# Kernel optimization log

Hardware: AMD Instinct MI355X
Metric: run time of the kernel (lower is better)

Reference implementation:

```python
import jax, jax.numpy as jnp
import numpy as np

N_NODES = 100000
N_EDGES = 1600000
F_IN = 64
F_HID = 64
F_OUT = 64
N_HEADS = 4


def setup_inputs() -> dict:
    key = jax.random.key(0)
    ks = jax.random.split(key, 7)
    h = jax.random.normal(ks[0], (N_NODES, F_IN), dtype=jnp.float32)
    src = jax.random.randint(ks[1], (N_EDGES,), 0, N_NODES, dtype=jnp.int32)
    dst = jax.random.randint(ks[2], (N_EDGES,), 0, N_NODES, dtype=jnp.int32)
    s = 1.0 / np.sqrt(F_IN)
    Wk = jax.random.normal(ks[3], (F_IN, F_HID), dtype=jnp.float32) * s
    Wq = jax.random.normal(ks[4], (F_IN, F_HID), dtype=jnp.float32) * s
    W = jax.random.normal(ks[5], (F_IN, F_OUT), dtype=jnp.float32) * s
    b = jnp.zeros((F_OUT,), dtype=jnp.float32)
    return {"h": h, "src": src, "dst": dst, "Wk": Wk, "Wq": Wq, "W": W, "b": b,
            "num_heads": N_HEADS}


def reference(h, src, dst, Wk, Wq, W, b, num_heads):
    N = h.shape[0]
    H = num_heads
    # k, q: [N, H, Dh]
    k = (h @ Wk).reshape(N, H, -1)
    q = (h @ Wq).reshape(N, H, -1)
    # edge scores e[e,h] = <k[src], q[dst]>  (u_dot_v)
    e = jnp.einsum('ehd,ehd->eh', k[src], q[dst])  # [E, H]
    # edge softmax over incoming edges of each destination node (per head)
    m = jax.ops.segment_max(e, dst, num_segments=N)          # [N, H]
    m = jax.lax.stop_gradient(m)
    ex = jnp.exp(e - m[dst])                                  # [E, H]
    z = jax.ops.segment_sum(ex, dst, num_segments=N)          # [N, H]
    a = ex / z[dst]                                           # [E, H]
    # message m = u_mul_e(h, a): broadcast (F,) with (H,1) -> [E, H, F]; sum to dst
    msg = h[src][:, None, :] * a[:, :, None]                  # [E, H, F]
    hn = jax.ops.segment_sum(msg, dst, num_segments=N)        # [N, H, F]
    out = hn @ W + b                                          # [N, H, F_out]
    return out.reshape(N, -1)                                 # [N, H*F_out]
```

## Files before the change

### kernel.cpp

```cpp
#include <hip/hip_runtime.h>
#include <hip/hip_fp16.h>
#include <math.h>


#define FDIM 64
#define NHEADS 4
#define TILE 8192
#define BCAP 6144

typedef float f32x2 __attribute__((ext_vector_type(2)));

__global__ __launch_bounds__(256) void k1_kernel(
    const float* __restrict__ h, const float* __restrict__ Wk,
    const float* __restrict__ Wq, const float* __restrict__ Wo,
    const int* __restrict__ src, const int* __restrict__ dst,
    __half* __restrict__ k16, __half* __restrict__ q16,
    __half* __restrict__ hp16, int* __restrict__ gcnt,
    unsigned int* __restrict__ ebuf,
    int N, int E, int KQB, int PB, int nbuck)
{
    __shared__ __align__(16) unsigned char smem_raw[39936];
    int bid = blockIdx.x;
    int t = threadIdx.x;
    if (bid < KQB) {
        float* sWk = (float*)smem_raw;
        float* sWq = (float*)(smem_raw + 16384);
        for (int i = t; i < FDIM * FDIM; i += 256) {
            sWk[i] = Wk[i] * 1.4426950408889634f;
            sWq[i] = Wq[i];
        }
        __syncthreads();
        int cg = t & 3;
        int rg = t >> 2;
        long base = (long)bid * 128 + rg * 2;
        const float4* sWk4 = (const float4*)sWk;
        const float4* sWq4 = (const float4*)sWq;
        const float4* h4 = (const float4*)h;
        float acck[2][16], accq[2][16];
#pragma unroll
        for (int i = 0; i < 2; ++i)
#pragma unroll
            for (int c = 0; c < 16; ++c) { acck[i][c] = 0.f; accq[i][c] = 0.f; }

        for (int fs = 0; fs < FDIM; fs += 4) {
            float4 hv[2];
#pragma unroll
            for (int i = 0; i < 2; ++i) {
                long r = base + i; if (r >= N) r = N - 1;
                hv[i] = h4[r * 16 + (fs >> 2)];
            }
#pragma unroll
            for (int fi = 0; fi < 4; ++fi) {
                int f = fs + fi;
                float4 wk0 = sWk4[f * 16 + cg * 4 + 0];
                float4 wk1 = sWk4[f * 16 + cg * 4 + 1];
                float4 wk2 = sWk4[f * 16 + cg * 4 + 2];
                float4 wk3 = sWk4[f * 16 + cg * 4 + 3];
                float4 wq0 = sWq4[f * 16 + cg * 4 + 0];
                float4 wq1 = sWq4[f * 16 + cg * 4 + 1];
                float4 wq2 = sWq4[f * 16 + cg * 4 + 2];
                float4 wq3 = sWq4[f * 16 + cg * 4 + 3];
#pragma unroll
                for (int i = 0; i < 2; ++i) {
                    float hvf = (&hv[i].x)[fi];
                    acck[i][0]  = fmaf(hvf, wk0.x, acck[i][0]);
                    acck[i][1]  = fmaf(hvf, wk0.y, acck[i][1]);
                    acck[i][2]  = fmaf(hvf, wk0.z, acck[i][2]);
                    acck[i][3]  = fmaf(hvf, wk0.w, acck[i][3]);
                    acck[i][4]  = fmaf(hvf, wk1.x, acck[i][4]);
                    acck[i][5]  = fmaf(hvf, wk1.y, acck[i][5]);
                    acck[i][6]  = fmaf(hvf, wk1.z, acck[i][6]);
                    acck[i][7]  = fmaf(hvf, wk1.w, acck[i][7]);
                    acck[i][8]  = fmaf(hvf, wk2.x, acck[i][8]);
                    acck[i][9]  = fmaf(hvf, wk2.y, acck[i][9]);
                    acck[i][10] = fmaf(hvf, wk2.z, acck[i][10]);
                    acck[i][11] = fmaf(hvf, wk2.w, acck[i][11]);
                    acck[i][12] = fmaf(hvf, wk3.x, acck[i][12]);
                    acck[i][13] = fmaf(hvf, wk3.y, acck[i][13]);
                    acck[i][14] = fmaf(hvf, wk3.z, acck[i][14]);
                    acck[i][15] = fmaf(hvf, wk3.w, acck[i][15]);
                    accq[i][0]  = fmaf(hvf, wq0.x, accq[i][0]);
                    accq[i][1]  = fmaf(hvf, wq0.y, accq[i][1]);
                    accq[i][2]  = fmaf(hvf, wq0.z, accq[i][2]);
                    accq[i][3]  = fmaf(hvf, wq0.w, accq[i][3]);
                    accq[i][4]  = fmaf(hvf, wq1.x, accq[i][4]);
                    accq[i][5]  = fmaf(hvf, wq1.y, accq[i][5]);
                    accq[i][6]  = fmaf(hvf, wq1.z, accq[i][6]);
                    accq[i][7]  = fmaf(hvf, wq1.w, accq[i][7]);
                    accq[i][8]  = fmaf(hvf, wq2.x, accq[i][8]);
                    accq[i][9]  = fmaf(hvf, wq2.y, accq[i][9]);
                    accq[i][10] = fmaf(hvf, wq2.z, accq[i][10]);
                    accq[i][11] = fmaf(hvf, wq2.w, accq[i][11]);
                    accq[i][12] = fmaf(hvf, wq3.x, accq[i][12]);
                    accq[i][13] = fmaf(hvf, wq3.y, accq[i][13]);
                    accq[i][14] = fmaf(hvf, wq3.z, accq[i][14]);
                    accq[i][15] = fmaf(hvf, wq3.w, accq[i][15]);
                }
            }
        }
#pragma unroll
        for (int i = 0; i < 2; ++i) {
            long r = base + i;
            if (r >= N) continue;
            __half2 hk[8], hq[8];
#pragma unroll
            for (int c = 0; c < 8; ++c) {
                hk[c] = __floats2half2_rn(acck[i][2 * c], acck[i][2 * c + 1]);
                hq[c] = __floats2half2_rn(accq[i][2 * c], accq[i][2 * c + 1]);
            }
            float4* kout = (float4*)(k16 + (size_t)r * FDIM + cg * 16);
            float4* qout = (float4*)(q16 + (size_t)r * FDIM + cg * 16);
            kout[0] = ((float4*)hk)[0]; kout[1] = ((float4*)hk)[1];
            qout[0] = ((float4*)hq)[0]; qout[1] = ((float4*)hq)[1];
        }
    } else if (bid < KQB + PB) {
        float* sW = (float*)smem_raw;
        for (int i = t; i < FDIM * FDIM; i += 256) sW[i] = Wo[i];
        __syncthreads();
        int cg = t & 3;
        int rg = t >> 2;
        long base = (long)(bid - KQB) * 128 + rg * 2;
        const float4* sW4 = (const float4*)sW;
        const float4* h4 = (const float4*)h;
        float accp[2][16];
#pragma unroll
        for (int i = 0; i < 2; ++i)
#pragma unroll
            for (int c = 0; c < 16; ++c) accp[i][c] = 0.f;

        for (int fs = 0; fs < FDIM; fs += 4) {
            float4 hv[2];
#pragma unroll
            for (int i = 0; i < 2; ++i) {
                long r = base + i; if (r >= N) r = N - 1;
                hv[i] = h4[r * 16 + (fs >> 2)];
            }
#pragma unroll
            for (int fi = 0; fi < 4; ++fi) {
                int f = fs + fi;
                float4 w0 = sW4[f * 16 + cg * 4 + 0];
                float4 w1 = sW4[f * 16 + cg * 4 + 1];
                float4 w2 = sW4[f * 16 + cg * 4 + 2];
                float4 w3 = sW4[f * 16 + cg * 4 + 3];
#pragma unroll
                for (int i = 0; i < 2; ++i) {
                    float hvf = (&hv[i].x)[fi];
                    accp[i][0]  = fmaf(hvf, w0.x, accp[i][0]);
                    accp[i][1]  = fmaf(hvf, w0.y, accp[i][1]);
                    accp[i][2]  = fmaf(hvf, w0.z, accp[i][2]);
                    accp[i][3]  = fmaf(hvf, w0.w, accp[i][3]);
                    accp[i][4]  = fmaf(hvf, w1.x, accp[i][4]);
                    accp[i][5]  = fmaf(hvf, w1.y, accp[i][5]);
                    accp[i][6]  = fmaf(hvf, w1.z, accp[i][6]);
                    accp[i][7]  = fmaf(hvf, w1.w, accp[i][7]);
                    accp[i][8]  = fmaf(hvf, w2.x, accp[i][8]);
                    accp[i][9]  = fmaf(hvf, w2.y, accp[i][9]);
                    accp[i][10] = fmaf(hvf, w2.z, accp[i][10]);
                    accp[i][11] = fmaf(hvf, w2.w, accp[i][11]);
                    accp[i][12] = fmaf(hvf, w3.x, accp[i][12]);
                    accp[i][13] = fmaf(hvf, w3.y, accp[i][13]);
                    accp[i][14] = fmaf(hvf, w3.z, accp[i][14]);
                    accp[i][15] = fmaf(hvf, w3.w, accp[i][15]);
                }
            }
        }
#pragma unroll
        for (int i = 0; i < 2; ++i) {
            long r = base + i;
            if (r >= N) continue;
            __half2 hp[8];
#pragma unroll
            for (int c = 0; c < 8; ++c)
                hp[c] = __floats2half2_rn(accp[i][2 * c], accp[i][2 * c + 1]);
            float4* pout = (float4*)(hp16 + (size_t)r * FDIM + cg * 16);
            pout[0] = ((float4*)hp)[0];
            pout[1] = ((float4*)hp)[1];
        }
    } else {
        unsigned int* bh     = (unsigned int*)smem_raw;
        unsigned int* bstart = bh + 512;
        unsigned int* bbase  = bstart + 512;
        unsigned int* sd     = bbase + 512;
        unsigned int* ebuf_l = sd + 256;
        long e0 = (long)(bid - KQB - PB) * TILE;
        int cnt_tile = (int)(((long)E - e0 < (long)TILE) ? ((long)E - e0) : (long)TILE);

        bh[t] = 0; bh[t + 256] = 0;
        __syncthreads();
        for (int j = t; j < cnt_tile; j += 256)
            atomicAdd(&bh[dst[e0 + j] >> 8], 1u);
        __syncthreads();
        unsigned int c0 = bh[2 * t], c1 = bh[2 * t + 1];
        unsigned int s = c0 + c1;
        sd[t] = s;
        __syncthreads();
        for (int off = 1; off < 256; off <<= 1) {
            unsigned int v = (t >= off) ? sd[t - off] : 0;
            __syncthreads();
            sd[t] += v;
            __syncthreads();
        }
        unsigned int ex = sd[t] - s;
        bh[2 * t] = ex;          bstart[2 * t] = ex;
        bh[2 * t + 1] = ex + c0; bstart[2 * t + 1] = ex + c0;
        if (c0 > 0) bbase[2 * t] = (unsigned int)atomicAdd(&gcnt[2 * t], (int)c0);
        if (c1 > 0) bbase[2 * t + 1] = (unsigned int)atomicAdd(&gcnt[2 * t + 1], (int)c1);
        __syncthreads();
        for (int j = t; j < cnt_tile; j += 256) {
            int d = dst[e0 + j];
            int sv = src[e0 + j];
            unsigned int pos = atomicAdd(&bh[d >> 8], 1u);
            ebuf_l[pos] = ((unsigned int)sv << 8) | (unsigned int)(d & 255);
        }
        __syncthreads();
        int wave = t >> 6, lane = t & 63;
        for (int b = wave; b < nbuck; b += 4) {
            unsigned int st = bstart[b];
            unsigned int en = bh[b];
            if (st == en) continue;
            unsigned int gb = bbase[b];
            if (gb >= (unsigned int)BCAP) continue;
            unsigned int room = (unsigned int)BCAP - gb;
            if (en - st > room) en = st + room;
            unsigned int* dstp = ebuf + (size_t)b * BCAP + gb;
            for (unsigned int j = st + lane; j < en; j += 64)
                dstp[j - st] = ebuf_l[j];
        }
    }
}

__global__ __launch_bounds__(1024) void binB_kernel(
    const int* __restrict__ gcnt, const unsigned int* __restrict__ ebuf,
    int* __restrict__ rowptr, int* __restrict__ srcs, int N)
{
    __shared__ int sg[512];
    __shared__ unsigned int lh[256];
    __shared__ unsigned int sd[256];
    __shared__ unsigned int ebuf_l[BCAP];
    __shared__ unsigned int srcs_l[BCAP];
    int t = threadIdx.x;
    int b = blockIdx.x;

    int c0 = 0, c1 = 0;
    if (t < 256) {
        c0 = gcnt[2 * t]; c1 = gcnt[2 * t + 1];
        sd[t] = (unsigned int)(c0 + c1);
        lh[t] = 0;
    }
    __syncthreads();
    for (int off = 1; off < 256; off <<= 1) {
        unsigned int v = (t < 256 && t >= off) ? sd[t - off] : 0;
        __syncthreads();
        if (t < 256) sd[t] += v;
        __syncthreads();
    }
    if (t < 256) {
        int ex = (int)sd[t] - (c0 + c1);
        sg[2 * t] = ex;
        sg[2 * t + 1] = ex + c0;
    }
    __syncthreads();
    int gb = sg[b];
    int cnt = gcnt[b];
    if (cnt > BCAP) cnt = BCAP;
    int n0 = b << 8;
    const unsigned int* eb = ebuf + (size_t)b * BCAP;

    for (int j = t; j < cnt; j += 1024) {
        unsigned int p = eb[j];
        ebuf_l[j] = p;
        atomicAdd(&lh[p & 255u], 1u);
    }
    __syncthreads();
    unsigned int c = 0;
    if (t < 256) { c = lh[t]; sd[t] = c; }
    __syncthreads();
    for (int off = 1; off < 256; off <<= 1) {
        unsigned int v = (t < 256 && t >= off) ? sd[t - off] : 0;
        __syncthreads();
        if (t < 256) sd[t] += v;
        __syncthreads();
    }
    if (t < 256) {
        unsigned int excl = sd[t] - c;
        lh[t] = excl;
        if (n0 + t < N) rowptr[n0 + t] = gb + (int)excl;
    }
    __syncthreads();
    for (int j = t; j < cnt; j += 1024) {
        unsigned int p = ebuf_l[j];
        unsigned int pos = atomicAdd(&lh[p & 255u], 1u);
        srcs_l[pos] = p >> 8;
    }
    __syncthreads();
    for (int j = t; j < cnt; j += 1024)
        srcs[gb + j] = (int)srcs_l[j];
}

__device__ __forceinline__ float dot16(const float4* kk, const float* qf) {
    const __half2* kh = (const __half2*)kk;
    float acc = 0.f;
#pragma unroll
    for (int j = 0; j < 8; ++j) {
        float2 kf = __half22float2(kh[j]);
        acc = fmaf(kf.x, qf[2 * j], acc);
        acc = fmaf(kf.y, qf[2 * j + 1], acc);
    }
    return acc;
}

__global__ __launch_bounds__(256) void fused_sa_kernel(
    const int* __restrict__ rowptr, const int* __restrict__ srcs,
    const __half* __restrict__ k16, const __half* __restrict__ q16,
    const __half* __restrict__ hp16, const float* __restrict__ bvec,
    float* __restrict__ out, int N, int E)
{
    int lane = threadIdx.x & 63;
    int n = blockIdx.x * 4 + (threadIdx.x >> 6);
    if (n >= N) return;
    int start = rowptr[n];
    int end   = (n == N - 1) ? E : rowptr[n + 1];

    int hh = lane & 3;
    int rr = lane >> 2;
    int qt = lane >> 4;
    int fq = lane & 15;

    const float4* qp = (const float4*)(q16 + (size_t)n * FDIM + hh * 16);
    float4 qv[2] = { qp[0], qp[1] };
    const __half2* qh = (const __half2*)qv;
    float qf[16];
#pragma unroll
    for (int j = 0; j < 8; ++j) {
        float2 f = __half22float2(qh[j]);
        qf[2 * j] = f.x;
        qf[2 * j + 1] = f.y;
    }

    float zacc = 0.f;
    f32x2 a00 = {0.f,0.f}, a01 = {0.f,0.f};
    f32x2 a10 = {0.f,0.f}, a11 = {0.f,0.f};
    f32x2 a20 = {0.f,0.f}, a21 = {0.f,0.f};
    f32x2 a30 = {0.f,0.f}, a31 = {0.f,0.f};

    for (int base = start; base < end; base += 16) {
        int idx = base + rr;
        bool valid = (idx < end);
        int ic = valid ? idx : (end - 1);
        int sA = srcs[ic];
        int sB0 = __shfl(sA, 4 * qt,      64);
        int sB1 = __shfl(sA, 16 + 4 * qt, 64);
        int sB2 = __shfl(sA, 32 + 4 * qt, 64);
        int sB3 = __shfl(sA, 48 + 4 * qt, 64);
        const float4* kp = (const float4*)(k16 + (size_t)sA * FDIM + hh * 16);
        float4 ka0 = kp[0], ka1 = kp[1];
        uint2 g0 = *(const uint2*)(hp16 + (size_t)sB0 * FDIM + fq * 4);
        uint2 g1 = *(const uint2*)(hp16 + (size_t)sB1 * FDIM + fq * 4);
        uint2 g2 = *(const uint2*)(hp16 + (size_t)sB2 * FDIM + fq * 4);
        uint2 g3 = *(const uint2*)(hp16 + (size_t)sB3 * FDIM + fq * 4);

        float4 ka[2] = { ka0, ka1 };
        float w = __builtin_amdgcn_exp2f(dot16(ka, qf));
        w = valid ? w : 0.f;
        zacc += w;

#define GRP(G, LBASE)                                                      \
    {   float w0 = __shfl(w, (LBASE) + 0, 64);                             \
        float w1 = __shfl(w, (LBASE) + 1, 64);                             \
        float w2 = __shfl(w, (LBASE) + 2, 64);                             \
        float w3 = __shfl(w, (LBASE) + 3, 64);                             \
        float2 flo = __half22float2(*(__half2*)&(G).x);                    \
        float2 fhi = __half22float2(*(__half2*)&(G).y);                    \
        f32x2 vlo; vlo.x = flo.x; vlo.y = flo.y;                           \
        f32x2 vhi; vhi.x = fhi.x; vhi.y = fhi.y;                           \
        f32x2 wv;                                                          \
        wv.x = w0; wv.y = w0;                                              \
        a00 = __builtin_elementwise_fma(wv, vlo, a00);                     \
        a01 = __builtin_elementwise_fma(wv, vhi, a01);                     \
        wv.x = w1; wv.y = w1;                                              \
        a10 = __builtin_elementwise_fma(wv, vlo, a10);                     \
        a11 = __builtin_elementwise_fma(wv, vhi, a11);                     \
        wv.x = w2; wv.y = w2;                                              \
        a20 = __builtin_elementwise_fma(wv, vlo, a20);                     \
        a21 = __builtin_elementwise_fma(wv, vhi, a21);                     \
        wv.x = w3; wv.y = w3;                                              \
        a30 = __builtin_elementwise_fma(wv, vlo, a30);                     \
        a31 = __builtin_elementwise_fma(wv, vhi, a31);                     }

        GRP(g0, 4 * qt)
        if (base + 4 < end)  { GRP(g1, 16 + 4 * qt) }
        if (base + 8 < end)  { GRP(g2, 32 + 4 * qt) }
        if (base + 12 < end) { GRP(g3, 48 + 4 * qt) }
#undef GRP
    }

    zacc += __shfl_xor(zacc, 4, 64);
    zacc += __shfl_xor(zacc, 8, 64);
    zacc += __shfl_xor(zacc, 16, 64);
    zacc += __shfl_xor(zacc, 32, 64);
    float z0 = __shfl(zacc, 0, 64);
    float z1 = __shfl(zacc, 1, 64);
    float z2 = __shfl(zacc, 2, 64);
    float z3 = __shfl(zacc, 3, 64);

#define MQ(A) \
    (A).x += __shfl_xor((A).x, 16, 64); (A).y += __shfl_xor((A).y, 16, 64); \
    (A).x += __shfl_xor((A).x, 32, 64); (A).y += __shfl_xor((A).y, 32, 64);
    MQ(a00) MQ(a01) MQ(a10) MQ(a11) MQ(a20) MQ(a21) MQ(a30) MQ(a31)
#undef MQ

    if (qt != 0) return;
    float4 bv = *(const float4*)(bvec + fq * 4);
    float4* o = (float4*)(out + (size_t)n * (NHEADS * FDIM));
    if (end > start) {
        float rz0 = 1.f / z0;
        float rz1 = 1.f / z1;
        float rz2 = 1.f / z2;
        float rz3 = 1.f / z3;
        o[fq] = make_float4(fmaf(a00.x, rz0, bv.x), fmaf(a00.y, rz0, bv.y),
                            fmaf(a01.x, rz0, bv.z), fmaf(a01.y, rz0, bv.w));
        o[16 + fq] = make_float4(fmaf(a10.x, rz1, bv.x), fmaf(a10.y, rz1, bv.y),
                                 fmaf(a11.x, rz1, bv.z), fmaf(a11.y, rz1, bv.w));
        o[32 + fq] = make_float4(fmaf(a20.x, rz2, bv.x), fmaf(a20.y, rz2, bv.y),
                                 fmaf(a21.x, rz2, bv.z), fmaf(a21.y, rz2, bv.w));
        o[48 + fq] = make_float4(fmaf(a30.x, rz3, bv.x), fmaf(a30.y, rz3, bv.y),
                                 fmaf(a31.x, rz3, bv.z), fmaf(a31.y, rz3, bv.w));
    } else {
        o[fq] = bv; o[16 + fq] = bv; o[32 + fq] = bv; o[48 + fq] = bv;
    }
}

extern "C" void kernel_launch(void* const* d_in, const int* in_sizes, int n_in,
                              void* d_out, int out_size, void* d_ws, size_t ws_size,
                              hipStream_t stream) {
    const float* h   = (const float*)d_in[0];
    const int*   src = (const int*)d_in[1];
    const int*   dst = (const int*)d_in[2];
    const float* Wk  = (const float*)d_in[3];
    const float* Wq  = (const float*)d_in[4];
    const float* W   = (const float*)d_in[5];
    const float* b   = (const float*)d_in[6];
    float* out = (float*)d_out;

    const int N = in_sizes[0] / FDIM;
    const int E = in_sizes[1];

    const int NBUCK = (N + 255) >> 8;
    const int NTILE = (E + TILE - 1) / TILE;
    const int KQB   = (N + 127) / 128;
    const int PB    = (N + 127) / 128;

    __half* k16 = (__half*)d_ws;
    __half* q16 = k16 + (size_t)N * FDIM;
    __half* hp16 = q16 + (size_t)N * FDIM;
    unsigned int* ebuf = (unsigned int*)(hp16 + (size_t)N * FDIM);
    int* srcs   = (int*)(ebuf + (size_t)NBUCK * BCAP);
    int* gcnt   = srcs + E;
    int* rowptr = gcnt + 512;

    hipMemsetAsync(gcnt, 0, 512 * sizeof(int), stream);

    k1_kernel<<<KQB + PB + NTILE, 256, 0, stream>>>(
        h, Wk, Wq, W, src, dst, k16, q16, hp16, gcnt, ebuf,
        N, E, KQB, PB, NBUCK);
    binB_kernel<<<NBUCK, 1024, 0, stream>>>(gcnt, ebuf, rowptr, srcs, N);
    fused_sa_kernel<<<(N + 3) / 4, 256, 0, stream>>>(
        rowptr, srcs, k16, q16, hp16, b, out, N, E);
}
```

Before: 315.0 us.

## Process four destination nodes per wavefront in fused attention kernel

```diff
diff --git a/kernel.cpp b/kernel.cpp
--- a/kernel.cpp
+++ b/kernel.cpp
@@ -316,17 +316,21 @@
     float* __restrict__ out, int N, int E)
 {
     int lane = threadIdx.x & 63;
-    int n = blockIdx.x * 4 + (threadIdx.x >> 6);
-    if (n >= N) return;
-    int start = rowptr[n];
-    int end   = (n == N - 1) ? E : rowptr[n + 1];
-
-    int hh = lane & 3;
-    int rr = lane >> 2;
+    int wid = threadIdx.x >> 6;
     int qt = lane >> 4;
-    int fq = lane & 15;
-
-    const float4* qp = (const float4*)(q16 + (size_t)n * FDIM + hh * 16);
+    int ql = lane & 15;
+    int n = blockIdx.x * 16 + wid * 4 + qt;
+    bool nvalid = (n < N);
+    int nc = nvalid ? n : N - 1;
+    int start = rowptr[nc];
+    int end = (nc == N - 1) ? E : rowptr[nc + 1];
+    if (!nvalid) end = start;
+
+    int rr = ql >> 2;
+    int hh = ql & 3;
+    int qb = qt * 16;
+
+    const float4* qp = (const float4*)(q16 + (size_t)nc * FDIM + hh * 16);
     float4 qv[2] = { qp[0], qp[1] };
     const __half2* qh = (const __half2*)qv;
     float qf[16];
@@ -343,21 +347,21 @@
     f32x2 a20 = {0.f,0.f}, a21 = {0.f,0.f};
     f32x2 a30 = {0.f,0.f}, a31 = {0.f,0.f};
 
-    for (int base = start; base < end; base += 16) {
+    for (int base = start; base < end; base += 4) {
         int idx = base + rr;
         bool valid = (idx < end);
         int ic = valid ? idx : (end - 1);
         int sA = srcs[ic];
-        int sB0 = __shfl(sA, 4 * qt,      64);
-        int sB1 = __shfl(sA, 16 + 4 * qt, 64);
-        int sB2 = __shfl(sA, 32 + 4 * qt, 64);
-        int sB3 = __shfl(sA, 48 + 4 * qt, 64);
+        int s0 = __shfl(sA, qb + 0,  64);
+        int s1 = __shfl(sA, qb + 4,  64);
+        int s2 = __shfl(sA, qb + 8,  64);
+        int s3 = __shfl(sA, qb + 12, 64);
         const float4* kp = (const float4*)(k16 + (size_t)sA * FDIM + hh * 16);
         float4 ka0 = kp[0], ka1 = kp[1];
-        uint2 g0 = *(const uint2*)(hp16 + (size_t)sB0 * FDIM + fq * 4);
-        uint2 g1 = *(const uint2*)(hp16 + (size_t)sB1 * FDIM + fq * 4);
-        uint2 g2 = *(const uint2*)(hp16 + (size_t)sB2 * FDIM + fq * 4);
-        uint2 g3 = *(const uint2*)(hp16 + (size_t)sB3 * FDIM + fq * 4);
+        uint2 g0 = *(const uint2*)(hp16 + (size_t)s0 * FDIM + ql * 4);
+        uint2 g1 = *(const uint2*)(hp16 + (size_t)s1 * FDIM + ql * 4);
+        uint2 g2 = *(const uint2*)(hp16 + (size_t)s2 * FDIM + ql * 4);
+        uint2 g3 = *(const uint2*)(hp16 + (size_t)s3 * FDIM + ql * 4);
 
         float4 ka[2] = { ka0, ka1 };
         float w = __builtin_amdgcn_exp2f(dot16(ka, qf));
@@ -387,46 +391,38 @@
         a30 = __builtin_elementwise_fma(wv, vlo, a30);                     \
         a31 = __builtin_elementwise_fma(wv, vhi, a31);                     }
 
-        GRP(g0, 4 * qt)
-        if (base + 4 < end)  { GRP(g1, 16 + 4 * qt) }
-        if (base + 8 < end)  { GRP(g2, 32 + 4 * qt) }
-        if (base + 12 < end) { GRP(g3, 48 + 4 * qt) }
+        GRP(g0, qb + 0)
+        if (base + 1 < end) { GRP(g1, qb + 4) }
+        if (base + 2 < end) { GRP(g2, qb + 8) }
+        if (base + 3 < end) { GRP(g3, qb + 12) }
 #undef GRP
     }
 
     zacc += __shfl_xor(zacc, 4, 64);
     zacc += __shfl_xor(zacc, 8, 64);
-    zacc += __shfl_xor(zacc, 16, 64);
-    zacc += __shfl_xor(zacc, 32, 64);
-    float z0 = __shfl(zacc, 0, 64);
-    float z1 = __shfl(zacc, 1, 64);
-    float z2 = __shfl(zacc, 2, 64);
-    float z3 = __shfl(zacc, 3, 64);
-
-#define MQ(A) \
-    (A).x += __shfl_xor((A).x, 16, 64); (A).y += __shfl_xor((A).y, 16, 64); \
-    (A).x += __shfl_xor((A).x, 32, 64); (A).y += __shfl_xor((A).y, 32, 64);
-    MQ(a00) MQ(a01) MQ(a10) MQ(a11) MQ(a20) MQ(a21) MQ(a30) MQ(a31)
-#undef MQ
-
-    if (qt != 0) return;
-    float4 bv = *(const float4*)(bvec + fq * 4);
+    float z0 = __shfl(zacc, qb + 0, 64);
+    float z1 = __shfl(zacc, qb + 1, 64);
+    float z2 = __shfl(zacc, qb + 2, 64);
+    float z3 = __shfl(zacc, qb + 3, 64);
+
+    if (!nvalid) return;
+    float4 bv = *(const float4*)(bvec + ql * 4);
     float4* o = (float4*)(out + (size_t)n * (NHEADS * FDIM));
     if (end > start) {
         float rz0 = 1.f / z0;
         float rz1 = 1.f / z1;
         float rz2 = 1.f / z2;
         float rz3 = 1.f / z3;
-        o[fq] = make_float4(fmaf(a00.x, rz0, bv.x), fmaf(a00.y, rz0, bv.y),
-                            fmaf(a01.x, rz0, bv.z), fmaf(a01.y, rz0, bv.w));
-        o[16 + fq] = make_float4(fmaf(a10.x, rz1, bv.x), fmaf(a10.y, rz1, bv.y),
+        o[ql]      = make_float4(fmaf(a00.x, rz0, bv.x), fmaf(a00.y, rz0, bv.y),
+                                 fmaf(a01.x, rz0, bv.z), fmaf(a01.y, rz0, bv.w));
+        o[16 + ql] = make_float4(fmaf(a10.x, rz1, bv.x), fmaf(a10.y, rz1, bv.y),
                                  fmaf(a11.x, rz1, bv.z), fmaf(a11.y, rz1, bv.w));
-        o[32 + fq] = make_float4(fmaf(a20.x, rz2, bv.x), fmaf(a20.y, rz2, bv.y),
+        o[32 + ql] = make_float4(fmaf(a20.x, rz2, bv.x), fmaf(a20.y, rz2, bv.y),
                                  fmaf(a21.x, rz2, bv.z), fmaf(a21.y, rz2, bv.w));
-        o[48 + fq] = make_float4(fmaf(a30.x, rz3, bv.x), fmaf(a30.y, rz3, bv.y),
+        o[48 + ql] = make_float4(fmaf(a30.x, rz3, bv.x), fmaf(a30.y, rz3, bv.y),
                                  fmaf(a31.x, rz3, bv.z), fmaf(a31.y, rz3, bv.w));
     } else {
-        o[fq] = bv; o[16 + fq] = bv; o[32 + fq] = bv; o[48 + fq] = bv;
+        o[ql] = bv; o[16 + ql] = bv; o[32 + ql] = bv; o[48 + ql] = bv;
     }
 }
 
@@ -464,6 +460,6 @@
         h, Wk, Wq, W, src, dst, k16, q16, hp16, gcnt, ebuf,
         N, E, KQB, PB, NBUCK);
     binB_kernel<<<NBUCK, 1024, 0, stream>>>(gcnt, ebuf, rowptr, srcs, N);
-    fused_sa_kernel<<<(N + 3) / 4, 256, 0, stream>>>(
+    fused_sa_kernel<<<(N + 15) / 16, 256, 0, stream>>>(
         rowptr, srcs, k16, q16, hp16, b, out, N, E);
 }
```

Measured after the change: 294.8 us. 1.07x faster.
